# Performance work log

Hardware: AMD Instinct MI355X
Metric: run time of the kernel (lower is better)

## Reference

```python
import jax, jax.numpy as jnp
import numpy as np
import math

T, NF, DF = 215, 36, 215      # timesteps, sensor nodes, GIN feature dim
D_PE, D_MODEL = 28, 64
BN_EPS = 1e-5


def _bn_eval(x, gamma, beta, mean, var):
    return (x - mean) * jax.lax.rsqrt(var + BN_EPS) * gamma + beta


def _gin(x, src_i, tgt_i, w1, b1, gamma, beta, mean, var, w2, b2):
    # GINConv (eps=0): nn(x + sum_{j->i} x_j); scatter-add over edge list
    agg = jax.ops.segment_sum(x[src_i], tgt_i, num_segments=x.shape[0])
    h = x + agg
    h = jax.nn.relu(_bn_eval(h @ w1 + b1, gamma, beta, mean, var))
    return jax.nn.relu(h @ w2 + b2)


def _edge_index(adj):
    # adj.triu() + adj.triu(1).T -> symmetric; nonzero (dense w.p. 1 -> 1296)
    adj_sym = jnp.triu(adj) + jnp.triu(adj, 1).T
    rows, cols = jnp.nonzero(adj_sym, size=NF * NF, fill_value=0)
    # direct edges (rows->cols targets per PyG flow) then inverse edges appended
    src_i = jnp.concatenate([rows, cols])
    tgt_i = jnp.concatenate([cols, rows])
    return src_i, tgt_i


def _pos_encode(times):
    # PositionalEncodingTF with d_pe=28 -> 14 timescales, base max_len=215
    ts = jnp.asarray(float(T) ** np.linspace(0.0, 1.0, D_PE // 2), dtype=times.dtype)
    scaled = times[..., None] / ts                      # [T,B,14]
    return jnp.concatenate([jnp.sin(scaled), jnp.cos(scaled)], axis=-1)  # [T,B,28]


def setup_inputs() -> dict:
    key = jax.random.key(0)
    ks = jax.random.split(key, 24)
    B = 4096
    f32 = jnp.float32
    rn = lambda k, s, sc=1.0: jax.random.normal(k, s, dtype=f32) * sc
    inp = {
        'src': rn(ks[0], (T, B, NF)),
        'static': rn(ks[1], (B, 9)),
        'times': jax.random.uniform(ks[2], (T, B), dtype=f32) * float(T),
        'lengths': jax.random.randint(ks[3], (B,), 1, T, dtype=jnp.int32),
        'adj': rn(ks[4], (NF, NF), math.sqrt(6.0 / (NF + NF))),
        'enc_w': rn(ks[5], (NF, NF), 0.05), 'enc_b': jnp.zeros((NF,), f32),
        'emb_w': rn(ks[6], (9, D_MODEL), 0.05), 'emb_b': jnp.zeros((D_MODEL,), f32),
        'mlp_w1': rn(ks[7], (D_MODEL, D_MODEL), 0.1), 'mlp_b1': jnp.zeros((D_MODEL,), f32),
        'mlp_w2': rn(ks[8], (D_MODEL, 2), 0.1), 'mlp_b2': jnp.zeros((2,), f32),
    }
    for i, pfx in enumerate(['g1', 'g2']):
        kk = jax.random.split(ks[9 + i], 4)
        inp[pfx + '_w1'] = rn(kk[0], (DF, DF), 0.05)
        inp[pfx + '_b1'] = jnp.zeros((DF,), f32)
        inp[pfx + '_gamma'] = 1.0 + rn(kk[1], (DF,), 0.1)
        inp[pfx + '_beta'] = rn(kk[2], (DF,), 0.1)
        inp[pfx + '_mean'] = jnp.zeros((DF,), f32)
        inp[pfx + '_var'] = jnp.ones((DF,), f32)
        inp[pfx + '_w2'] = rn(kk[3], (DF, DF), 0.05)
        inp[pfx + '_b2'] = jnp.zeros((DF,), f32)
    return inp


def reference(src, static, times, lengths, adj, enc_w, enc_b, emb_w, emb_b,
              g1_w1, g1_b1, g1_gamma, g1_beta, g1_mean, g1_var, g1_w2, g1_b2,
              g2_w1, g2_b1, g2_gamma, g2_beta, g2_mean, g2_var, g2_w2, g2_b2,
              mlp_w1, mlp_b1, mlp_w2, mlp_b2):
    maxlen, B = src.shape[0], src.shape[1]
    # encoder + scale (dropout is identity in eval)
    h = (src @ enc_w + enc_b) * math.sqrt(float(D_MODEL))          # [T,B,36]
    pe = _pos_encode(times)                                        # [T,B,28]
    emb = static @ emb_w + emb_b                                   # [B,64]
    src_i, tgt_i = _edge_index(adj)
    # GIN over flattened node rows; edges only touch nodes 0..35 (as in source)
    x = h.transpose(1, 2, 0).reshape(-1, DF)                       # [B*36,215]
    x = _gin(x, src_i, tgt_i, g1_w1, g1_b1, g1_gamma, g1_beta, g1_mean, g1_var, g1_w2, g1_b2)
    x = _gin(x, src_i, tgt_i, g2_w1, g2_b1, g2_gamma, g2_beta, g2_mean, g2_var, g2_w2, g2_b2)
    out = x.reshape(-1, NF, DF).transpose(2, 0, 1)                 # [215,B,36]
    out = jnp.concatenate([pe, out], axis=2)                       # [215,B,64]
    full = jnp.concatenate([emb[None], out], axis=0)               # [216,B,64]
    # mask rows past lengths+1, mean-aggregate over time
    mask = jnp.arange(maxlen + 1)[None, :] >= (lengths[:, None] + 1)  # [B,216]
    w = (1.0 - mask.T[..., None].astype(full.dtype))               # [216,B,1]
    agg = jnp.sum(full * w, axis=0) / (lengths[:, None] + 1).astype(full.dtype)
    return jax.nn.relu(agg @ mlp_w1 + mlp_b1) @ mlp_w2 + mlp_b2    # [B,2]
```

## Files before the change

### kernel.cpp

```cpp
#include <hip/hip_runtime.h>
#include <math.h>

#define T_LEN 215
#define BATCH 4096
#define NFEAT 36
#define DF 215
#define KP 224
#define NROWS (BATCH*NFEAT)
#define WP 256
#define WROWS 224
#define WELEMS (WROWS*WP)

typedef __bf16 v8bf __attribute__((ext_vector_type(8)));
typedef float f32x16 __attribute__((ext_vector_type(16)));

static __device__ __forceinline__ float bf2f(ushort u) {
    return __uint_as_float(((uint)u) << 16);
}
static __device__ __forceinline__ ushort f2bf(float f) {
    uint x = __float_as_uint(f);
    return (ushort)((x + 0x7FFFu + ((x >> 16) & 1u)) >> 16);
}

__global__ __launch_bounds__(256) void wprep_kernel(
    const float* __restrict__ w1a, const float* __restrict__ w2a,
    const float* __restrict__ w1b, const float* __restrict__ w2b,
    ushort* __restrict__ wt)
{
    const float* src = (blockIdx.z == 0) ? w1a : (blockIdx.z == 1) ? w2a
                     : (blockIdx.z == 2) ? w1b : w2b;
    ushort* dst = wt + (size_t)blockIdx.z * WELEMS;
    __shared__ float tile[32][33];
    int k0 = blockIdx.x * 32, h0 = blockIdx.y * 32;
    int j = threadIdx.x & 31, i0 = threadIdx.x >> 5;
    for (int i = i0; i < 32; i += 8) {
        int k = k0 + i, h = h0 + j;
        tile[i][j] = (k < DF && h < DF) ? src[(size_t)k * DF + h] : 0.f;
    }
    __syncthreads();
    for (int i = i0; i < 32; i += 8) {
        int h = h0 + i;
        int ks = (k0 + j) ^ ((h & 7) << 3);
        dst[(size_t)h * WP + ks] = f2bf(tile[j][i]);
    }
    if (blockIdx.x == 6) {
        for (int i = i0; i < 32; i += 8) {
            int h = h0 + i;
            int ks = (224 + j) ^ ((h & 7) << 3);
            dst[(size_t)h * WP + ks] = 0;
        }
    }
}

__global__ __launch_bounds__(256) void enc_kernel(const float* __restrict__ src,
    const float* __restrict__ enc_w, const float* __restrict__ enc_b,
    ushort* __restrict__ X0, float* __restrict__ S)
{
    __shared__ float st[T_LEN * NFEAT];
    int tid = threadIdx.x;
    int b   = blockIdx.x;

    for (int i = tid; i < T_LEN * 9; i += 256) {
        int t = i / 9, q = i - t * 9;
        *(float4*)&st[t*NFEAT + q*4] =
            *(const float4*)(src + ((size_t)t*BATCH + b)*NFEAT + q*4);
    }
    __syncthreads();

    int t = tid;
    if (t < KP) {
        float acc[NFEAT];
        if (t < T_LEN) {
            float x[NFEAT];
            #pragma unroll
            for (int q = 0; q < 9; ++q)
                *(float4*)&x[q*4] = *(const float4*)&st[t*NFEAT + q*4];
            #pragma unroll
            for (int n = 0; n < NFEAT; ++n) acc[n] = enc_b[n];
            #pragma unroll 4
            for (int m = 0; m < NFEAT; ++m) {
                float xm = x[m];
                #pragma unroll
                for (int n = 0; n < NFEAT; ++n)
                    acc[n] = fmaf(xm, enc_w[m*NFEAT + n], acc[n]);
            }
            #pragma unroll
            for (int n = 0; n < NFEAT; ++n) acc[n] *= 8.0f;
        } else {
            #pragma unroll
            for (int n = 0; n < NFEAT; ++n) acc[n] = 0.f;
        }
        size_t base = (size_t)b * NFEAT * KP;
        #pragma unroll
        for (int n = 0; n < NFEAT; ++n)
            X0[base + (size_t)n*KP + t] = f2bf(acc[n]);
        if (b == 0) {
            float s = 0.f;
            #pragma unroll
            for (int n = 0; n < NFEAT; ++n) s += acc[n];
            S[t] = 2.0f * s;
        }
    }
}

__global__ void colsum_kernel(const ushort* __restrict__ X, float* __restrict__ S)
{
    int t = threadIdx.x;
    if (t < KP) {
        float s = 0.f;
        #pragma unroll
        for (int n = 0; n < NFEAT; ++n) s += bf2f(X[n*KP + t]);
        S[t] = 2.0f * s;
    }
}

__global__ __launch_bounds__(512, 1) void gin_mfma_kernel(
    ushort* __restrict__ X, const float* __restrict__ S2,
    const ushort* __restrict__ Wt1, const ushort* __restrict__ Wt2,
    const float* __restrict__ B1v, const float* __restrict__ Gm,
    const float* __restrict__ Bt,  const float* __restrict__ Mn,
    const float* __restrict__ Vr,  const float* __restrict__ B2v)
{
    __shared__ ushort wlds[WELEMS];
    __shared__ float bnsc[224], bnsh[224], b2s[224];

    int tid  = threadIdx.x;
    int lane = tid & 63, wv = tid >> 6;
    int ml   = lane & 31, half = lane >> 5;
    int row  = blockIdx.x * 256 + wv * 32 + ml;

    if (tid < 224) {
        if (tid < DF) {
            float sc = Gm[tid] * rsqrtf(Vr[tid] + 1e-5f);
            bnsc[tid] = sc;
            bnsh[tid] = fmaf(B1v[tid] - Mn[tid], sc, Bt[tid]);
            b2s[tid]  = B2v[tid];
        } else { bnsc[tid] = 0.f; bnsh[tid] = 0.f; b2s[tid] = 0.f; }
    }
    {
        const uint4* s = (const uint4*)Wt1;
        uint4* d = (uint4*)wlds;
        for (int i = tid; i < WELEMS/8; i += 512) d[i] = s[i];
    }

    ushort* xr = X + (size_t)row * KP;
    bool agg = row < NFEAT;
    uint4 B1[14];
    #pragma unroll
    for (int kb = 0; kb < 14; ++kb) {
        uint4 r = *(const uint4*)(xr + kb*16 + half*8);
        if (agg) {
            int k0 = kb*16 + half*8;
            uint w0 = r.x, w1 = r.y, w2 = r.z, w3 = r.w;
            float a0 = bf2f((ushort)(w0 & 0xffff)) + S2[k0+0];
            float a1 = bf2f((ushort)(w0 >> 16))    + S2[k0+1];
            float a2 = bf2f((ushort)(w1 & 0xffff)) + S2[k0+2];
            float a3 = bf2f((ushort)(w1 >> 16))    + S2[k0+3];
            float a4 = bf2f((ushort)(w2 & 0xffff)) + S2[k0+4];
            float a5 = bf2f((ushort)(w2 >> 16))    + S2[k0+5];
            float a6 = bf2f((ushort)(w3 & 0xffff)) + S2[k0+6];
            float a7 = bf2f((ushort)(w3 >> 16))    + S2[k0+7];
            r.x = ((uint)f2bf(a1) << 16) | f2bf(a0);
            r.y = ((uint)f2bf(a3) << 16) | f2bf(a2);
            r.z = ((uint)f2bf(a5) << 16) | f2bf(a4);
            r.w = ((uint)f2bf(a7) << 16) | f2bf(a6);
        }
        B1[kb] = r;
    }
    __syncthreads();

    uint4 B2[14];
    #pragma unroll
    for (int ht = 0; ht < 7; ++ht) {
        f32x16 acc;
        #pragma unroll
        for (int r = 0; r < 16; ++r) acc[r] = 0.f;
        #pragma unroll
        for (int kb = 0; kb < 14; ++kb) {
            int rrow = ht*32 + ml;
            int by = rrow*512 + ((kb*32 + half*16) ^ ((rrow & 7) << 4));
            uint4 a = *(const uint4*)((const char*)wlds + by);
            acc = __builtin_amdgcn_mfma_f32_32x32x16_bf16(
                      __builtin_bit_cast(v8bf, a),
                      __builtin_bit_cast(v8bf, B1[kb]), acc, 0, 0, 0);
        }
        int hb = ht*32;
        uint d[8];
        #pragma unroll
        for (int p = 0; p < 8; ++p) {
            int r0 = 2*p;
            int h0i = hb + (r0 & 3) + 8*(r0 >> 2) + 4*half;
            float v0 = fmaxf(fmaf(acc[r0],   bnsc[h0i],   bnsh[h0i]),   0.f);
            float v1 = fmaxf(fmaf(acc[r0+1], bnsc[h0i+1], bnsh[h0i+1]), 0.f);
            d[p] = ((uint)f2bf(v1) << 16) | f2bf(v0);
        }
        uint ea = __shfl_xor(half ? d[0] : d[2], 32);
        uint eb = __shfl_xor(half ? d[1] : d[3], 32);
        uint ec = __shfl_xor(half ? d[4] : d[6], 32);
        uint ed = __shfl_xor(half ? d[5] : d[7], 32);
        B2[2*ht]   = half ? make_uint4(ea, eb, d[2], d[3])
                          : make_uint4(d[0], d[1], ea, eb);
        B2[2*ht+1] = half ? make_uint4(ec, ed, d[6], d[7])
                          : make_uint4(d[4], d[5], ec, ed);
    }
    __syncthreads();
    {
        const uint4* s = (const uint4*)Wt2;
        uint4* d = (uint4*)wlds;
        for (int i = tid; i < WELEMS/8; i += 512) d[i] = s[i];
    }
    __syncthreads();

    #pragma unroll
    for (int nt = 0; nt < 7; ++nt) {
        f32x16 acc;
        #pragma unroll
        for (int r = 0; r < 16; ++r) acc[r] = 0.f;
        #pragma unroll
        for (int kb = 0; kb < 14; ++kb) {
            int rrow = nt*32 + ml;
            int by = rrow*512 + ((kb*32 + half*16) ^ ((rrow & 7) << 4));
            uint4 a = *(const uint4*)((const char*)wlds + by);
            acc = __builtin_amdgcn_mfma_f32_32x32x16_bf16(
                      __builtin_bit_cast(v8bf, a),
                      __builtin_bit_cast(v8bf, B2[kb]), acc, 0, 0, 0);
        }
        int nb = nt*32;
        #pragma unroll
        for (int g = 0; g < 4; ++g) {
            int r0 = 4*g;
            int n0 = nb + 8*g + 4*half;
            float v0 = fmaxf(acc[r0]   + b2s[n0],   0.f);
            float v1 = fmaxf(acc[r0+1] + b2s[n0+1], 0.f);
            float v2 = fmaxf(acc[r0+2] + b2s[n0+2], 0.f);
            float v3 = fmaxf(acc[r0+3] + b2s[n0+3], 0.f);
            uint lo = ((uint)f2bf(v1) << 16) | f2bf(v0);
            uint hi = ((uint)f2bf(v3) << 16) | f2bf(v2);
            if (n0 + 3 < DF) {
                *(uint2*)(xr + n0) = make_uint2(lo, hi);
            } else {
                if (n0     < DF) xr[n0]     = (ushort)(lo & 0xffff);
                if (n0 + 1 < DF) xr[n0 + 1] = (ushort)(lo >> 16);
                if (n0 + 2 < DF) xr[n0 + 2] = (ushort)(hi & 0xffff);
            }
        }
    }
}

__device__ inline float wave_sum(float v) {
    #pragma unroll
    for (int off = 32; off > 0; off >>= 1) v += __shfl_down(v, off);
    return v;
}

__global__ __launch_bounds__(256) void final_kernel(const ushort* __restrict__ Y2,
    const float* __restrict__ times, const int* __restrict__ lengths,
    const float* __restrict__ stat, const float* __restrict__ emb_w,
    const float* __restrict__ emb_b, const float* __restrict__ w1,
    const float* __restrict__ b1, const float* __restrict__ w2,
    const float* __restrict__ b2, float* __restrict__ out)
{
    int b = blockIdx.x, tid = threadIdx.x;
    int lane = tid & 63, w = tid >> 6;
    int L = lengths[b];
    __shared__ float aggs[64];
    __shared__ float red[4][28];
    __shared__ float hsh[64];

    #pragma unroll
    for (int q = 0; q < 9; ++q) {
        int n = w*9 + q;
        const ushort* row = Y2 + (size_t)(b*NFEAT + n)*KP;
        float s = 0.f;
        for (int t = lane; t < L; t += 64) s += bf2f(row[t]);
        s = wave_sum(s);
        if (lane == 0) aggs[28 + n] = s;
    }

    float psin[14], pcos[14];
    #pragma unroll
    for (int k = 0; k < 14; ++k) { psin[k] = 0.f; pcos[k] = 0.f; }
    if (tid < L) {
        float x = times[(size_t)tid*BATCH + b];
        #pragma unroll
        for (int k = 0; k < 14; ++k) {
            float arg = x * exp2f(-0.59601508f * (float)k);
            float s, c;
            sincosf(arg, &s, &c);
            psin[k] = s; pcos[k] = c;
        }
    }
    #pragma unroll
    for (int k = 0; k < 14; ++k) {
        float v = wave_sum(psin[k]);
        if (lane == 0) red[w][k] = v;
        v = wave_sum(pcos[k]);
        if (lane == 0) red[w][14 + k] = v;
    }
    __syncthreads();
    if (tid < 28) aggs[tid] = red[0][tid] + red[1][tid] + red[2][tid] + red[3][tid];
    __syncthreads();

    if (tid < 64) {
        float e = emb_b[tid];
        #pragma unroll
        for (int m = 0; m < 9; ++m) e = fmaf(stat[b*9 + m], emb_w[m*64 + tid], e);
        aggs[tid] = (aggs[tid] + e) / (float)(L + 1);
    }
    __syncthreads();

    if (tid < 64) {
        float a = b1[tid];
        #pragma unroll
        for (int f = 0; f < 64; ++f) a = fmaf(aggs[f], w1[f*64 + tid], a);
        hsh[tid] = fmaxf(a, 0.f);
    }
    __syncthreads();
    if (tid < 2) {
        float a = b2[tid];
        #pragma unroll
        for (int j = 0; j < 64; ++j) a = fmaf(hsh[j], w2[j*2 + tid], a);
        out[b*2 + tid] = a;
    }
}

extern "C" void kernel_launch(void* const* d_in, const int* in_sizes, int n_in,
                              void* d_out, int out_size, void* d_ws, size_t ws_size,
                              hipStream_t stream)
{
    const float* src     = (const float*)d_in[0];
    const float* stat    = (const float*)d_in[1];
    const float* times   = (const float*)d_in[2];
    const int*   lengths = (const int*)  d_in[3];
    const float* enc_w   = (const float*)d_in[5];
    const float* enc_b   = (const float*)d_in[6];
    const float* emb_w   = (const float*)d_in[7];
    const float* emb_b   = (const float*)d_in[8];
    const float* mlp_w1  = (const float*)d_in[9];
    const float* mlp_b1  = (const float*)d_in[10];
    const float* mlp_w2  = (const float*)d_in[11];
    const float* mlp_b2  = (const float*)d_in[12];
    const float* g1_w1   = (const float*)d_in[13];
    const float* g1_b1   = (const float*)d_in[14];
    const float* g1_gm   = (const float*)d_in[15];
    const float* g1_bt   = (const float*)d_in[16];
    const float* g1_mn   = (const float*)d_in[17];
    const float* g1_vr   = (const float*)d_in[18];
    const float* g1_w2   = (const float*)d_in[19];
    const float* g1_b2   = (const float*)d_in[20];
    const float* g2_w1   = (const float*)d_in[21];
    const float* g2_b1   = (const float*)d_in[22];
    const float* g2_gm   = (const float*)d_in[23];
    const float* g2_bt   = (const float*)d_in[24];
    const float* g2_mn   = (const float*)d_in[25];
    const float* g2_vr   = (const float*)d_in[26];
    const float* g2_w2   = (const float*)d_in[27];
    const float* g2_b2   = (const float*)d_in[28];

    ushort* X0 = (ushort*)d_ws;
    ushort* Wt = X0 + (size_t)NROWS * KP;
    float*  S  = (float*)(Wt + 4 * (size_t)WELEMS);

    wprep_kernel<<<dim3(7, 7, 4), 256, 0, stream>>>(g1_w1, g1_w2, g2_w1, g2_w2, Wt);
    enc_kernel<<<BATCH, 256, 0, stream>>>(src, enc_w, enc_b, X0, S);

    gin_mfma_kernel<<<NROWS/256, 512, 0, stream>>>(X0, S, Wt, Wt + WELEMS,
        g1_b1, g1_gm, g1_bt, g1_mn, g1_vr, g1_b2);

    colsum_kernel<<<1, 256, 0, stream>>>(X0, S);
    gin_mfma_kernel<<<NROWS/256, 512, 0, stream>>>(X0, S, Wt + 2*WELEMS, Wt + 3*WELEMS,
        g2_b1, g2_gm, g2_bt, g2_mn, g2_vr, g2_b2);

    final_kernel<<<BATCH, 256, 0, stream>>>(X0, times, lengths, stat, emb_w, emb_b,
                                            mlp_w1, mlp_b1, mlp_w2, mlp_b2,
                                            (float*)d_out);
}
```

Measured before the change: 524.2 us.

## Read GIN weights directly from global, shrink blocks, precompute BN, coalesce stores

The GIN MFMA kernel stops staging the swizzled weight matrices in LDS with 512-thread blocks. It now runs one-wave blocks that read the unswizzled weights straight from global memory, relying on the cache, and the BN scale/shift vectors are computed once by a new small kernel. The encoder kernel stages its output in shared memory so it can be written to global with coalesced 16-byte stores. The final kernel reads each node row as vectorized uint4 loads with a half-wave reduction instead of strided scalar loads. This removes LDS fill and barrier costs and raises occupancy, at the risk of heavier global and cache traffic for the weight operand.

```diff
diff --git a/kernel.cpp b/kernel.cpp
--- a/kernel.cpp
+++ b/kernel.cpp
@@ -7,9 +7,8 @@
 #define DF 215
 #define KP 224
 #define NROWS (BATCH*NFEAT)
-#define WP 256
-#define WROWS 224
-#define WELEMS (WROWS*WP)
+#define WP 224
+#define WELEMS (WP*WP)
 
 typedef __bf16 v8bf __attribute__((ext_vector_type(8)));
 typedef float f32x16 __attribute__((ext_vector_type(16)));
@@ -38,18 +37,34 @@
         tile[i][j] = (k < DF && h < DF) ? src[(size_t)k * DF + h] : 0.f;
     }
     __syncthreads();
-    for (int i = i0; i < 32; i += 8) {
-        int h = h0 + i;
-        int ks = (k0 + j) ^ ((h & 7) << 3);
-        dst[(size_t)h * WP + ks] = f2bf(tile[j][i]);
-    }
-    if (blockIdx.x == 6) {
-        for (int i = i0; i < 32; i += 8) {
-            int h = h0 + i;
-            int ks = (224 + j) ^ ((h & 7) << 3);
-            dst[(size_t)h * WP + ks] = 0;
-        }
-    }
+    for (int i = i0; i < 32; i += 8)
+        dst[(size_t)(h0 + i) * WP + k0 + j] = f2bf(tile[j][i]);
+}
+
+__global__ void bnprep_kernel(
+    const float* __restrict__ b1a, const float* __restrict__ gma,
+    const float* __restrict__ bta, const float* __restrict__ mna,
+    const float* __restrict__ vra, const float* __restrict__ b2a,
+    const float* __restrict__ b1b, const float* __restrict__ gmb,
+    const float* __restrict__ btb, const float* __restrict__ mnb,
+    const float* __restrict__ vrb, const float* __restrict__ b2b,
+    float* __restrict__ bn)
+{
+    int z = blockIdx.x, t = threadIdx.x;
+    const float* B1 = z ? b1b : b1a;
+    const float* Gm = z ? gmb : gma;
+    const float* Bt = z ? btb : bta;
+    const float* Mn = z ? mnb : mna;
+    const float* Vr = z ? vrb : vra;
+    const float* B2 = z ? b2b : b2a;
+    float sc = 0.f, sh = 0.f, bb = 0.f;
+    if (t < DF) {
+        sc = Gm[t] * rsqrtf(Vr[t] + 1e-5f);
+        sh = fmaf(B1[t] - Mn[t], sc, Bt[t]);
+        bb = B2[t];
+    }
+    float* o = bn + z * 672;
+    o[t] = sc; o[224 + t] = sh; o[448 + t] = bb;
 }
 
 __global__ __launch_bounds__(256) void enc_kernel(const float* __restrict__ src,
@@ -57,6 +72,7 @@
     ushort* __restrict__ X0, float* __restrict__ S)
 {
     __shared__ float st[T_LEN * NFEAT];
+    __shared__ ushort sx[NFEAT * KP];
     int tid = threadIdx.x;
     int b   = blockIdx.x;
 
@@ -90,10 +106,8 @@
             #pragma unroll
             for (int n = 0; n < NFEAT; ++n) acc[n] = 0.f;
         }
-        size_t base = (size_t)b * NFEAT * KP;
-        #pragma unroll
-        for (int n = 0; n < NFEAT; ++n)
-            X0[base + (size_t)n*KP + t] = f2bf(acc[n]);
+        #pragma unroll
+        for (int n = 0; n < NFEAT; ++n) sx[n*KP + t] = f2bf(acc[n]);
         if (b == 0) {
             float s = 0.f;
             #pragma unroll
@@ -101,6 +115,11 @@
             S[t] = 2.0f * s;
         }
     }
+    __syncthreads();
+
+    uint4* dst = (uint4*)(X0 + (size_t)b * NFEAT * KP);
+    const uint4* s4 = (const uint4*)sx;
+    for (int i = tid; i < NFEAT*KP/8; i += 256) dst[i] = s4[i];
 }
 
 __global__ void colsum_kernel(const ushort* __restrict__ X, float* __restrict__ S)
@@ -114,34 +133,14 @@
     }
 }
 
-__global__ __launch_bounds__(512, 1) void gin_mfma_kernel(
+__global__ __launch_bounds__(64) void gin_mfma_kernel(
     ushort* __restrict__ X, const float* __restrict__ S2,
     const ushort* __restrict__ Wt1, const ushort* __restrict__ Wt2,
-    const float* __restrict__ B1v, const float* __restrict__ Gm,
-    const float* __restrict__ Bt,  const float* __restrict__ Mn,
-    const float* __restrict__ Vr,  const float* __restrict__ B2v)
-{
-    __shared__ ushort wlds[WELEMS];
-    __shared__ float bnsc[224], bnsh[224], b2s[224];
-
-    int tid  = threadIdx.x;
-    int lane = tid & 63, wv = tid >> 6;
+    const float* __restrict__ bn)
+{
+    int lane = threadIdx.x;
     int ml   = lane & 31, half = lane >> 5;
-    int row  = blockIdx.x * 256 + wv * 32 + ml;
-
-    if (tid < 224) {
-        if (tid < DF) {
-            float sc = Gm[tid] * rsqrtf(Vr[tid] + 1e-5f);
-            bnsc[tid] = sc;
-            bnsh[tid] = fmaf(B1v[tid] - Mn[tid], sc, Bt[tid]);
-            b2s[tid]  = B2v[tid];
-        } else { bnsc[tid] = 0.f; bnsh[tid] = 0.f; b2s[tid] = 0.f; }
-    }
-    {
-        const uint4* s = (const uint4*)Wt1;
-        uint4* d = (uint4*)wlds;
-        for (int i = tid; i < WELEMS/8; i += 512) d[i] = s[i];
-    }
+    int row  = blockIdx.x * 32 + ml;
 
     ushort* xr = X + (size_t)row * KP;
     bool agg = row < NFEAT;
@@ -167,7 +166,6 @@
         }
         B1[kb] = r;
     }
-    __syncthreads();
 
     uint4 B2[14];
     #pragma unroll
@@ -175,11 +173,10 @@
         f32x16 acc;
         #pragma unroll
         for (int r = 0; r < 16; ++r) acc[r] = 0.f;
+        const ushort* wbase = Wt1 + (size_t)(ht*32 + ml)*WP + half*8;
         #pragma unroll
         for (int kb = 0; kb < 14; ++kb) {
-            int rrow = ht*32 + ml;
-            int by = rrow*512 + ((kb*32 + half*16) ^ ((rrow & 7) << 4));
-            uint4 a = *(const uint4*)((const char*)wlds + by);
+            uint4 a = *(const uint4*)(wbase + kb*16);
             acc = __builtin_amdgcn_mfma_f32_32x32x16_bf16(
                       __builtin_bit_cast(v8bf, a),
                       __builtin_bit_cast(v8bf, B1[kb]), acc, 0, 0, 0);
@@ -190,8 +187,8 @@
         for (int p = 0; p < 8; ++p) {
             int r0 = 2*p;
             int h0i = hb + (r0 & 3) + 8*(r0 >> 2) + 4*half;
-            float v0 = fmaxf(fmaf(acc[r0],   bnsc[h0i],   bnsh[h0i]),   0.f);
-            float v1 = fmaxf(fmaf(acc[r0+1], bnsc[h0i+1], bnsh[h0i+1]), 0.f);
+            float v0 = fmaxf(fmaf(acc[r0],   bn[h0i],       bn[224+h0i]),   0.f);
+            float v1 = fmaxf(fmaf(acc[r0+1], bn[h0i+1],     bn[224+h0i+1]), 0.f);
             d[p] = ((uint)f2bf(v1) << 16) | f2bf(v0);
         }
         uint ea = __shfl_xor(half ? d[0] : d[2], 32);
@@ -203,24 +200,16 @@
         B2[2*ht+1] = half ? make_uint4(ec, ed, d[6], d[7])
                           : make_uint4(d[4], d[5], ec, ed);
     }
-    __syncthreads();
-    {
-        const uint4* s = (const uint4*)Wt2;
-        uint4* d = (uint4*)wlds;
-        for (int i = tid; i < WELEMS/8; i += 512) d[i] = s[i];
-    }
-    __syncthreads();
 
     #pragma unroll
     for (int nt = 0; nt < 7; ++nt) {
         f32x16 acc;
         #pragma unroll
         for (int r = 0; r < 16; ++r) acc[r] = 0.f;
+        const ushort* wbase = Wt2 + (size_t)(nt*32 + ml)*WP + half*8;
         #pragma unroll
         for (int kb = 0; kb < 14; ++kb) {
-            int rrow = nt*32 + ml;
-            int by = rrow*512 + ((kb*32 + half*16) ^ ((rrow & 7) << 4));
-            uint4 a = *(const uint4*)((const char*)wlds + by);
+            uint4 a = *(const uint4*)(wbase + kb*16);
             acc = __builtin_amdgcn_mfma_f32_32x32x16_bf16(
                       __builtin_bit_cast(v8bf, a),
                       __builtin_bit_cast(v8bf, B2[kb]), acc, 0, 0, 0);
@@ -230,10 +219,10 @@
         for (int g = 0; g < 4; ++g) {
             int r0 = 4*g;
             int n0 = nb + 8*g + 4*half;
-            float v0 = fmaxf(acc[r0]   + b2s[n0],   0.f);
-            float v1 = fmaxf(acc[r0+1] + b2s[n0+1], 0.f);
-            float v2 = fmaxf(acc[r0+2] + b2s[n0+2], 0.f);
-            float v3 = fmaxf(acc[r0+3] + b2s[n0+3], 0.f);
+            float v0 = fmaxf(acc[r0]   + bn[448+n0],   0.f);
+            float v1 = fmaxf(acc[r0+1] + bn[448+n0+1], 0.f);
+            float v2 = fmaxf(acc[r0+2] + bn[448+n0+2], 0.f);
+            float v3 = fmaxf(acc[r0+3] + bn[448+n0+3], 0.f);
             uint lo = ((uint)f2bf(v1) << 16) | f2bf(v0);
             uint hi = ((uint)f2bf(v3) << 16) | f2bf(v2);
             if (n0 + 3 < DF) {
@@ -268,13 +257,24 @@
     __shared__ float hsh[64];
 
     #pragma unroll
-    for (int q = 0; q < 9; ++q) {
-        int n = w*9 + q;
-        const ushort* row = Y2 + (size_t)(b*NFEAT + n)*KP;
+    for (int p = 0; p < 5; ++p) {
+        int sub = lane >> 5, c = lane & 31;
+        int n = w*9 + 2*p + sub;
+        bool rowok = (2*p + sub) < 9;
         float s = 0.f;
-        for (int t = lane; t < L; t += 64) s += bf2f(row[t]);
-        s = wave_sum(s);
-        if (lane == 0) aggs[28 + n] = s;
+        if (rowok && c < 28) {
+            uint4 v = *(const uint4*)(Y2 + (size_t)(b*NFEAT + n)*KP + c*8);
+            int t0 = c*8;
+            uint arr[4] = {v.x, v.y, v.z, v.w};
+            #pragma unroll
+            for (int e = 0; e < 4; ++e) {
+                if (t0 + 2*e     < L) s += bf2f((ushort)(arr[e] & 0xffff));
+                if (t0 + 2*e + 1 < L) s += bf2f((ushort)(arr[e] >> 16));
+            }
+        }
+        #pragma unroll
+        for (int off = 16; off > 0; off >>= 1) s += __shfl_xor(s, off);
+        if ((lane & 31) == 0 && rowok) aggs[28 + n] = s;
     }
 
     float psin[14], pcos[14];
@@ -360,16 +360,18 @@
     ushort* X0 = (ushort*)d_ws;
     ushort* Wt = X0 + (size_t)NROWS * KP;
     float*  S  = (float*)(Wt + 4 * (size_t)WELEMS);
+    float*  BN = S + 224;
 
     wprep_kernel<<<dim3(7, 7, 4), 256, 0, stream>>>(g1_w1, g1_w2, g2_w1, g2_w2, Wt);
+    bnprep_kernel<<<2, 224, 0, stream>>>(g1_b1, g1_gm, g1_bt, g1_mn, g1_vr, g1_b2,
+                                         g2_b1, g2_gm, g2_bt, g2_mn, g2_vr, g2_b2, BN);
     enc_kernel<<<BATCH, 256, 0, stream>>>(src, enc_w, enc_b, X0, S);
 
-    gin_mfma_kernel<<<NROWS/256, 512, 0, stream>>>(X0, S, Wt, Wt + WELEMS,
-        g1_b1, g1_gm, g1_bt, g1_mn, g1_vr, g1_b2);
+    gin_mfma_kernel<<<NROWS/32, 64, 0, stream>>>(X0, S, Wt, Wt + WELEMS, BN);
 
     colsum_kernel<<<1, 256, 0, stream>>>(X0, S);
-    gin_mfma_kernel<<<NROWS/256, 512, 0, stream>>>(X0, S, Wt + 2*WELEMS, Wt + 3*WELEMS,
-        g2_b1, g2_gm, g2_bt, g2_mn, g2_vr, g2_b2);
+    gin_mfma_kernel<<<NROWS/32, 64, 0, stream>>>(X0, S, Wt + 2*WELEMS, Wt + 3*WELEMS,
+                                                 BN + 672);
 
     final_kernel<<<BATCH, 256, 0, stream>>>(X0, times, lengths, stat, emb_w, emb_b,
                                             mlp_w1, mlp_b1, mlp_w2, mlp_b2,
```

After: 607.6 us. 1.16x slower.
